# Optimization experiments

Measured on AMD Instinct MI355X. Metric: run time of the kernel, lower is better.

## Reference

```python
import jax, jax.numpy as jnp
import numpy as np
from jax import lax

THRESH = 0.6      # pnet score threshold (threshold[0])
IOU_THR = 0.5     # per-scale nms threshold in detect_face
K_PICKS = 128     # fixed max number of NMS picks (jit-static)
STRIDE = 2.0
CELL = 12.0
NEG = -1e30


def _conv(x, w, b):
    y = lax.conv_general_dilated(x, w, (1, 1), 'VALID',
                                 dimension_numbers=('NCHW', 'OIHW', 'NCHW'))
    return y + b[None, :, None, None]


def _prelu(x, a):
    return jnp.where(x > 0, x, a[None, :, None, None] * x)


def _maxpool2(x):
    return lax.reduce_window(x, -jnp.inf, lax.max, (1, 1, 2, 2), (1, 1, 2, 2), 'VALID')


def _nms(boxes, scores):
    # Greedy union-IoU NMS (nms_numpy math), vectorized with a fixed pick budget.
    # boxes [N,4] (shared grid), scores [N] with invalid entries already = NEG.
    x1, y1, x2, y2 = boxes[:, 0], boxes[:, 1], boxes[:, 2], boxes[:, 3]
    area = (x2 - x1 + 1.0) * (y2 - y1 + 1.0)

    def body(live, _):
        j = jnp.argmax(live)
        s = live[j]
        ok = s > NEG * 0.5
        xx1 = jnp.maximum(x1[j], x1); yy1 = jnp.maximum(y1[j], y1)
        xx2 = jnp.minimum(x2[j], x2); yy2 = jnp.minimum(y2[j], y2)
        inter = jnp.maximum(0.0, xx2 - xx1 + 1.0) * jnp.maximum(0.0, yy2 - yy1 + 1.0)
        iou = inter / (area[j] + area - inter)
        live = jnp.where(iou > IOU_THR, NEG, live).at[j].set(NEG)
        return live, (j, ok)

    _, (idx, ok) = lax.scan(body, scores, None, length=K_PICKS)
    return idx, ok


def setup_inputs():
    key = jax.random.key(0)
    ks = jax.random.split(key, 16)
    B, H, W = 16, 384, 512
    f = lambda k, shp, s=0.1: jax.random.normal(k, shp, jnp.float32) * s
    return {
        'im_data': jax.random.uniform(ks[0], (B, 3, H, W), jnp.float32) * 255.0,
        'c1_w': f(ks[1], (10, 3, 3, 3)), 'c1_b': f(ks[2], (10,)),
        'p1': jnp.full((10,), 0.25, jnp.float32),
        'c2_w': f(ks[3], (16, 10, 3, 3)), 'c2_b': f(ks[4], (16,)),
        'p2': jnp.full((16,), 0.25, jnp.float32),
        'c3_w': f(ks[5], (32, 16, 3, 3)), 'c3_b': f(ks[6], (32,)),
        'p3': jnp.full((32,), 0.25, jnp.float32),
        'c41_w': f(ks[7], (2, 32, 1, 1)), 'c41_b': f(ks[8], (2,)),
        'c42_w': f(ks[9], (4, 32, 1, 1)), 'c42_b': f(ks[10], (4,)),
    }


def reference(im_data, c1_w, c1_b, p1, c2_w, c2_b, p2, c3_w, c3_b, p3,
              c41_w, c41_b, c42_w, c42_b):
    # --- PNet conv trunk (detect_face normalization + MTCNN PNet) ---
    x = (im_data - 127.5) * 0.0078125
    h = _prelu(_conv(x, c1_w, c1_b), p1)
    h = _maxpool2(h)                                   # 2x2 s2 (dims even -> ceil==floor)
    h = _prelu(_conv(h, c2_w, c2_b), p2)
    h = _prelu(_conv(h, c3_w, c3_b), p3)
    probs = jax.nn.softmax(_conv(h, c41_w, c41_b), axis=1)[:, 1]   # [B,Hp,Wp]
    reg = _conv(h, c42_w, c42_b)                                   # [B,4,Hp,Wp]

    # --- generateBoundingBox (dense, masked instead of nonzero; scale=1) ---
    B, Hp, Wp = probs.shape
    yy, xx = jnp.meshgrid(jnp.arange(Hp, dtype=jnp.float32),
                          jnp.arange(Wp, dtype=jnp.float32), indexing='ij')
    boxes4 = jnp.stack([jnp.floor(STRIDE * xx + 1.0).ravel(),
                        jnp.floor(STRIDE * yy + 1.0).ravel(),
                        jnp.floor(STRIDE * xx + CELL).ravel(),
                        jnp.floor(STRIDE * yy + CELL).ravel()], axis=1)  # [N,4]
    scores = probs.reshape(B, -1)                                   # [B,N]
    regf = reg.reshape(B, 4, -1).transpose(0, 2, 1)                 # [B,N,4]
    masked = jnp.where(scores >= THRESH, scores, NEG)

    # --- per-image greedy NMS (batched_nms: images independent) ---
    idx, ok = jax.vmap(_nms, in_axes=(None, 0))(boxes4, masked)     # [B,K]
    pb = boxes4[idx]                                                # [B,K,4]
    ps = jnp.take_along_axis(scores, idx, axis=1)                   # [B,K]
    pr = jnp.take_along_axis(regf, idx[..., None], axis=1)          # [B,K,4]

    w = pb[..., 2] - pb[..., 0]
    hh = pb[..., 3] - pb[..., 1]
    q1 = pb[..., 0] + pr[..., 0] * w
    q2 = pb[..., 1] + pr[..., 1] * hh
    q3 = pb[..., 2] + pr[..., 2] * w
    q4 = pb[..., 3] + pr[..., 3] * hh
    rw = q3 - q1
    rh = q4 - q2
    l = jnp.maximum(rw, rh)
    nx1 = q1 + rw * 0.5 - l * 0.5
    ny1 = q2 + rh * 0.5 - l * 0.5
    out = jnp.stack([nx1, ny1, nx1 + l, ny1 + l, ps], axis=-1)      # [B,K,5]
    return out * ok[..., None].astype(out.dtype)
```

## Files before the change

kernel.cpp:

```cpp
#include <hip/hip_runtime.h>
#include <math.h>

#define BATCH 16
#define IH 384
#define IW 512
#define C1 10
#define P1H 191
#define P1W 255
#define C2 16
#define H2 189
#define W2 253
#define C3 32
#define H3 187
#define W3 251
#define N3 (H3*W3)
#define KP 128
#define CAP 7680
#define NEGV (-1e30f)

typedef _Float16 f16x8 __attribute__((ext_vector_type(8)));
typedef _Float16 f16x4 __attribute__((ext_vector_type(4)));
typedef float    f32x16 __attribute__((ext_vector_type(16)));

#define PXT 66
#define NSUB 2

#define T1R 34
#define T1C 68
__global__ __launch_bounds__(256, 1) void k_conv1pool(
        const float* __restrict__ im, const float* __restrict__ w,
        const float* __restrict__ bia, const float* __restrict__ slope,
        float* __restrict__ outp,
        const float* __restrict__ w3, _Float16* __restrict__ wbuf) {
    __shared__ float T[3 * T1R * T1C];

    int tx = threadIdx.x, ty = threadIdx.y;
    int tid = ty * 16 + tx;
    int bx = blockIdx.x, by = blockIdx.y, bb = blockIdx.z;

    if (bx == 0 && by == 0 && bb == 0) {
        for (int e = tid; e < 4608; e += 256) {
            int oc = e / 144;
            int rem = e - oc * 144;
            int ic = rem / 9;
            int tap = rem - ic * 9;
            float v = w3[e];
            _Float16 h = (_Float16)v;
            _Float16 l = (_Float16)(v - (float)h);
            int d = ((tap * 2 + (ic >> 3)) * 32 + oc) * 8 + (ic & 7);
            wbuf[d] = h;
            wbuf[4608 + d] = l;
        }
    }

    const size_t ibase = (size_t)bb * 3 * IH * IW;
    for (int g = tid; g < 3 * T1R * 33; g += 256) {
        int ch = g / (T1R * 33);
        int rem = g - ch * (T1R * 33);
        int r = rem / 33;
        int c2 = rem - r * 33;
        int yg = 32 * by + r;
        int xg = 64 * bx + 2 * c2;
        float2 v = make_float2(0.f, 0.f);
        if (yg < IH && xg < IW)
            v = *(const float2*)(im + ibase + ((size_t)ch * IH + yg) * IW + xg);
        float2 o;
        o.x = (v.x - 127.5f) * 0.0078125f;
        o.y = (v.y - 127.5f) * 0.0078125f;
        *(float2*)&T[(ch * T1R + r) * T1C + 2 * c2] = o;
    }
    __syncthreads();

    int Y  = by * 16 + ty;
    int X0 = bx * 32 + 2 * tx;
    if (Y >= P1H) return;

    float win[3][4][6];
    #pragma unroll
    for (int ch = 0; ch < 3; ++ch)
        #pragma unroll
        for (int r = 0; r < 4; ++r) {
            const float* p = &T[(ch * T1R + 2 * ty + r) * T1C + 4 * tx];
            float4 a = *(const float4*)p;
            float2 b = *(const float2*)(p + 4);
            win[ch][r][0] = a.x; win[ch][r][1] = a.y;
            win[ch][r][2] = a.z; win[ch][r][3] = a.w;
            win[ch][r][4] = b.x; win[ch][r][5] = b.y;
        }
    #pragma unroll
    for (int ch = 0; ch < 3; ++ch)
        #pragma unroll
        for (int r = 0; r < 4; ++r)
            #pragma unroll
            for (int c = 0; c < 6; ++c)
                asm volatile("" : "+v"(win[ch][r][c]));

    bool px1ok = (X0 + 1 < P1W);
    for (int oc = 0; oc < C1; ++oc) {
        const float* wo = w + oc * 27;
        float bv = bia[oc], sv = slope[oc];
        float c0 = bv, c1 = bv, c2 = bv, c3 = bv;
        float c4 = bv, c5 = bv, c6 = bv, c7 = bv;
        #pragma unroll
        for (int ch = 0; ch < 3; ++ch)
            #pragma unroll
            for (int ky = 0; ky < 3; ++ky)
                #pragma unroll
                for (int kx = 0; kx < 3; ++kx) {
                    float wv = wo[(ch * 3 + ky) * 3 + kx];
                    c0 += win[ch][0 + ky][0 + kx] * wv;
                    c1 += win[ch][0 + ky][1 + kx] * wv;
                    c2 += win[ch][0 + ky][2 + kx] * wv;
                    c3 += win[ch][0 + ky][3 + kx] * wv;
                    c4 += win[ch][1 + ky][0 + kx] * wv;
                    c5 += win[ch][1 + ky][1 + kx] * wv;
                    c6 += win[ch][1 + ky][2 + kx] * wv;
                    c7 += win[ch][1 + ky][3 + kx] * wv;
                }
        float m0 = fmaxf(fmaxf(c0, c1), fmaxf(c4, c5));
        float m1 = fmaxf(fmaxf(c2, c3), fmaxf(c6, c7));
        float p0 = m0 > 0.f ? m0 : sv * m0;
        float p1 = m1 > 0.f ? m1 : sv * m1;
        float* o = outp + (((size_t)bb * C1 + oc) * P1H + Y) * P1W + X0;
        o[0] = p0;
        if (px1ok) o[1] = p1;
    }
}

__global__ __launch_bounds__(256, 2) void k_conv2(
        const float* __restrict__ inp, const float* __restrict__ w,
        const float* __restrict__ bia, const float* __restrict__ slope,
        float* __restrict__ outp) {
    __shared__ __align__(16) float smem[8192];
    float* tile = smem;
    float4* sbuf = (float4*)smem;

    int tx = threadIdx.x, ty = threadIdx.y;
    int tid = ty * 64 + tx;
    int bx = blockIdx.x, byb = blockIdx.y, bb = blockIdx.z;

    const float* pin = inp + (size_t)bb * C1 * P1H * P1W;
    for (int g = tid; g < C1 * 6 * 130; g += 256) {
        int ic = g / 780;
        int rem = g - ic * 780;
        int r = rem / 130;
        int c = rem - r * 130;
        int yg = 4 * byb + r;
        int xg = 128 * bx + c;
        float v = 0.f;
        if (yg < P1H && xg < P1W)
            v = pin[((size_t)ic * P1H + yg) * P1W + xg];
        tile[(ic * 6 + r) * 132 + c] = v;
    }
    __syncthreads();

    int x0 = bx * 128 + tx * 2;
    int y  = byb * 4 + ty;
    bool alive = (x0 < W2) && (y < H2);

    float a0[C2], a1[C2];
    #pragma unroll
    for (int oc = 0; oc < C2; ++oc) { a0[oc] = bia[oc]; a1[oc] = bia[oc]; }

    if (alive) {
        for (int ci = 0; ci < C1; ++ci) {
            float v[3][4];
            #pragma unroll
            for (int r = 0; r < 3; ++r) {
                const float* p = &tile[(ci * 6 + ty + r) * 132 + 2 * tx];
                float2 u0 = *(const float2*)p;
                float2 u1 = *(const float2*)(p + 2);
                v[r][0] = u0.x; v[r][1] = u0.y; v[r][2] = u1.x; v[r][3] = u1.y;
            }
            const float* wc = w + ci * 9;
            #pragma unroll
            for (int oc = 0; oc < C2; ++oc) {
                const float* wo = wc + oc * (C1 * 9);
                float s0 = a0[oc], s1 = a1[oc];
                #pragma unroll
                for (int ky = 0; ky < 3; ++ky)
                    #pragma unroll
                    for (int kx = 0; kx < 3; ++kx) {
                        float wv = wo[ky * 3 + kx];
                        s0 += v[ky][kx]     * wv;
                        s1 += v[ky][kx + 1] * wv;
                    }
                a0[oc] = s0; a1[oc] = s1;
            }
        }
        #pragma unroll
        for (int oc = 0; oc < C2; ++oc) {
            float sl = slope[oc];
            float u0 = a0[oc]; a0[oc] = u0 > 0.f ? u0 : sl * u0;
            float u1 = a1[oc]; a1[oc] = u1 > 0.f ? u1 : sl * u1;
        }
    }
    __syncthreads();

    #pragma unroll
    for (int c4 = 0; c4 < 4; ++c4) {
        int g0 = tid * 8 + c4;
        int p0 = g0 ^ ((g0 >> 3) & 7);
        sbuf[p0] = make_float4(a0[c4 * 4], a0[c4 * 4 + 1], a0[c4 * 4 + 2], a0[c4 * 4 + 3]);
        int g1 = tid * 8 + 4 + c4;
        int p1 = g1 ^ ((g1 >> 3) & 7);
        sbuf[p1] = make_float4(a1[c4 * 4], a1[c4 * 4 + 1], a1[c4 * 4 + 2], a1[c4 * 4 + 3]);
    }
    __syncthreads();

    const size_t obase = (size_t)bb * H2 * W2 * C2;
    #pragma unroll
    for (int it = 0; it < 8; ++it) {
        int g = it * 256 + tid;
        int c4 = g & 3, px = (g >> 2) & 127, ry = g >> 9;
        int xg = blockIdx.x * 128 + px, yg = blockIdx.y * 4 + ry;
        if (xg < W2 && yg < H2) {
            int phys = g ^ ((g >> 3) & 7);
            *(float4*)(outp + obase + ((size_t)yg * W2 + xg) * C2 + c4 * 4) = sbuf[phys];
        }
    }
}

__global__ __launch_bounds__(256, 2) void k_conv3mfma(
        const float* __restrict__ act,
        const _Float16* __restrict__ wbuf,
        const float* __restrict__ b3, const float* __restrict__ s3,
        const float* __restrict__ w41, const float* __restrict__ b41,
        const float* __restrict__ w42, const float* __restrict__ b42,
        float* __restrict__ scores, float4* __restrict__ regf) {
    __shared__ __align__(16) _Float16 Ah[6 * 2 * PXT * 8];
    __shared__ __align__(16) _Float16 Al[6 * 2 * PXT * 8];
    __shared__ __align__(16) float    htab[32 * 8];

    int tid = threadIdx.x;
    int bx = blockIdx.x * (NSUB * 32);
    int by = blockIdx.y * 4;
    int bb = blockIdx.z;

    {
        int oc = tid >> 3, f = tid & 7;
        float v;
        if      (f == 0) v = b3[oc];
        else if (f == 1) v = s3[oc];
        else if (f == 2) v = w41[oc];
        else if (f == 3) v = w41[32 + oc];
        else             v = w42[(f - 4) * 32 + oc];
        htab[tid] = v;
    }
    {
        const float* actb = act + (size_t)bb * H2 * W2 * C2;
        for (int e = tid; e < 6 * PXT * 4; e += 256) {
            int ic4 = e & 3;
            int t = e >> 2;
            int px = t % PXT;
            int row = t / PXT;
            int yg = by + row, xg = bx + px;
            float4 v = make_float4(0.f, 0.f, 0.f, 0.f);
            if (yg < H2 && xg < W2)
                v = *(const float4*)(actb + ((size_t)yg * W2 + xg) * C2 + ic4 * 4);
            float xs0 = v.x, xs1 = v.y, xs2 = v.z, xs3 = v.w;
            f16x4 hv, lv;
            _Float16 h;
            h = (_Float16)xs0; hv[0] = h; lv[0] = (_Float16)(xs0 - (float)h);
            h = (_Float16)xs1; hv[1] = h; lv[1] = (_Float16)(xs1 - (float)h);
            h = (_Float16)xs2; hv[2] = h; lv[2] = (_Float16)(xs2 - (float)h);
            h = (_Float16)xs3; hv[3] = h; lv[3] = (_Float16)(xs3 - (float)h);
            int kg = ic4 >> 1, h4 = ic4 & 1;
            int gr = (row * 2 + kg) * PXT + px;
            *(f16x4*)(Ah + gr * 8 + h4 * 4) = hv;
            *(f16x4*)(Al + gr * 8 + h4 * 4) = lv;
        }
    }
    __syncthreads();

    int wv = tid >> 6, lane = tid & 63;
    int col = lane & 31, half = lane >> 5;
    int y = by + wv;
    if (y >= H3) return;

    f32x16 acc[NSUB];
    #pragma unroll
    for (int s = 0; s < NSUB; ++s)
        #pragma unroll
        for (int i = 0; i < 16; ++i) acc[s][i] = 0.f;

    const _Float16* wg = wbuf + (half * 32 + col) * 8;

    #pragma unroll 1
    for (int ky = 0; ky < 3; ++ky) {
        const _Float16* arh = Ah + ((wv + ky) * 2 + half) * (PXT * 8);
        const _Float16* arl = Al + ((wv + ky) * 2 + half) * (PXT * 8);
        #pragma unroll
        for (int kx = 0; kx < 3; ++kx) {
            int tap = ky * 3 + kx;
            f16x8 wh = *(const f16x8*)(wg + tap * 512);
            f16x8 wl = *(const f16x8*)(wg + 4608 + tap * 512);
            #pragma unroll
            for (int s = 0; s < NSUB; ++s) {
                int p = s * 32 + col + kx;
                f16x8 bh = *(const f16x8*)(arh + p * 8);
                f16x8 bl = *(const f16x8*)(arl + p * 8);
                acc[s] = __builtin_amdgcn_mfma_f32_32x32x16_f16(wh, bh, acc[s], 0, 0, 0);
                acc[s] = __builtin_amdgcn_mfma_f32_32x32x16_f16(wl, bh, acc[s], 0, 0, 0);
                acc[s] = __builtin_amdgcn_mfma_f32_32x32x16_f16(wh, bl, acc[s], 0, 0, 0);
            }
        }
    }

    float L0[NSUB], L1[NSUB], R0[NSUB], R1[NSUB], R2[NSUB], R3[NSUB];
    #pragma unroll
    for (int s = 0; s < NSUB; ++s) { L0[s]=0.f; L1[s]=0.f; R0[s]=0.f; R1[s]=0.f; R2[s]=0.f; R3[s]=0.f; }

    #pragma unroll
    for (int r = 0; r < 16; ++r) {
        int oc = (r & 3) + 8 * (r >> 2) + 4 * half;
        float4 t0 = *(const float4*)&htab[oc * 8];
        float4 t1 = *(const float4*)&htab[oc * 8 + 4];
        #pragma unroll
        for (int s = 0; s < NSUB; ++s) {
            float v = acc[s][r] + t0.x;
            v = v > 0.f ? v : v * t0.y;
            L0[s] += v * t0.z; L1[s] += v * t0.w;
            R0[s] += v * t1.x; R1[s] += v * t1.y;
            R2[s] += v * t1.z; R3[s] += v * t1.w;
        }
    }

    float hb0 = b41[0], hb1 = b41[1];
    float rb0 = b42[0], rb1 = b42[1], rb2 = b42[2], rb3 = b42[3];

    #pragma unroll
    for (int s = 0; s < NSUB; ++s) {
        float l0 = L0[s] + __shfl_xor(L0[s], 32) + hb0;
        float l1 = L1[s] + __shfl_xor(L1[s], 32) + hb1;
        float r0 = R0[s] + __shfl_xor(R0[s], 32) + rb0;
        float r1 = R1[s] + __shfl_xor(R1[s], 32) + rb1;
        float r2 = R2[s] + __shfl_xor(R2[s], 32) + rb2;
        float r3 = R3[s] + __shfl_xor(R3[s], 32) + rb3;
        float m = fmaxf(l0, l1);
        float e0 = expf(l0 - m), e1 = expf(l1 - m);
        float p = e1 / (e0 + e1);
        int px = bx + s * 32 + col;
        if (half == 0 && px < W3) {
            size_t n = (size_t)bb * N3 + (size_t)y * W3 + px;
            scores[n] = (p >= 0.6f) ? p : NEGV;
            regf[n] = make_float4(r0, r1, r2, r3);
        }
    }
}

__global__ __launch_bounds__(1024) void k_nms(
        const float* __restrict__ scores, const float4* __restrict__ regf,
        float* __restrict__ outp) {
    __shared__ float s_score[CAP];
    __shared__ int   s_idx[CAP];
    __shared__ float r_s[16];
    __shared__ int   r_i[16];
    __shared__ float s_picks[KP];
    __shared__ int   s_picki[KP];
    __shared__ int   s_misc[4];

    int tid = threadIdx.x;
    int bb = blockIdx.x;
    const float* sc = scores + (size_t)bb * N3;

    if (tid < 4) s_misc[tid] = 0;
    __syncthreads();

    int cnt = 0;
    for (int i = tid; i < N3; i += 1024) if (sc[i] > 0.f) cnt++;
    atomicAdd(&s_misc[0], cnt);
    __syncthreads();
    int M = s_misc[0];

    int cutbin = 0;
    if (M > CAP) {
        for (int i = tid; i < 2048; i += 1024) s_idx[i] = 0;
        __syncthreads();
        for (int i = tid; i < N3; i += 1024) {
            float s = sc[i];
            if (s > 0.f) {
                int b = (int)((s - 0.6f) * 5120.f);
                b = b < 0 ? 0 : (b > 2047 ? 2047 : b);
                atomicAdd(&s_idx[b], 1);
            }
        }
        __syncthreads();
        if (tid == 0) {
            int accum = 0, b = 2047;
            for (; b >= 0; --b) {
                int c = s_idx[b];
                if (accum + c > CAP) break;
                accum += c;
            }
            s_misc[2] = b + 1;
        }
        __syncthreads();
        cutbin = s_misc[2];
        __syncthreads();
    }

    for (int i = tid; i < N3; i += 1024) {
        float s = sc[i];
        if (s > 0.f) {
            bool keep = true;
            if (M > CAP) {
                int b = (int)((s - 0.6f) * 5120.f);
                b = b < 0 ? 0 : (b > 2047 ? 2047 : b);
                keep = (b >= cutbin);
            }
            if (keep) {
                int pos = atomicAdd(&s_misc[1], 1);
                if (pos < CAP) { s_score[pos] = s; s_idx[pos] = i; }
            }
        }
    }
    __syncthreads();
    int M2 = s_misc[1]; if (M2 > CAP) M2 = CAP;

    int np = 0;
    for (int pick = 0; pick < KP; ++pick) {
        float bs = -INFINITY; int bi = 0x7fffffff;
        for (int i = tid; i < M2; i += 1024) {
            float s = s_score[i]; int id = s_idx[i];
            if (s > bs || (s == bs && id < bi)) { bs = s; bi = id; }
        }
        #pragma unroll
        for (int off = 32; off; off >>= 1) {
            float os = __shfl_down(bs, off);
            int   oi = __shfl_down(bi, off);
            if (os > bs || (os == bs && oi < bi)) { bs = os; bi = oi; }
        }
        int lane = tid & 63, wv = tid >> 6;
        if (lane == 0) { r_s[wv] = bs; r_i[wv] = bi; }
        __syncthreads();
        if (tid == 0) {
            float ps = r_s[0]; int pi = r_i[0];
            for (int k = 1; k < 16; ++k) {
                float os = r_s[k]; int oi = r_i[k];
                if (os > ps || (os == ps && oi < pi)) { ps = os; pi = oi; }
            }
            s_picks[pick] = ps; s_picki[pick] = pi;
            r_s[0] = ps; r_i[0] = pi;
        }
        __syncthreads();
        float ps = r_s[0]; int pi = r_i[0];
        if (ps < 0.f) break;
        np = pick + 1;

        int pcx = pi % W3, pcy = pi / W3;
        float px1 = (float)(2 * pcx + 1), py1 = (float)(2 * pcy + 1);
        float px2 = (float)(2 * pcx + 12), py2 = (float)(2 * pcy + 12);
        for (int i = tid; i < M2; i += 1024) {
            float s = s_score[i];
            if (s > NEGV * 0.5f) {
                int id = s_idx[i];
                int cx = id % W3, cy = id / W3;
                float x1 = (float)(2 * cx + 1), y1 = (float)(2 * cy + 1);
                float x2 = (float)(2 * cx + 12), y2 = (float)(2 * cy + 12);
                float xx1 = fmaxf(px1, x1), yy1 = fmaxf(py1, y1);
                float xx2 = fminf(px2, x2), yy2 = fminf(py2, y2);
                float inter = fmaxf(0.f, xx2 - xx1 + 1.f) * fmaxf(0.f, yy2 - yy1 + 1.f);
                float iou = inter / (288.f - inter);
                if (iou > 0.5f) s_score[i] = NEGV;
            }
        }
        __syncthreads();
    }

    if (tid < KP) {
        float* o = outp + ((size_t)bb * KP + tid) * 5;
        if (tid < np) {
            int pi = s_picki[tid]; float ps = s_picks[tid];
            int cx = pi % W3, cy = pi / W3;
            float x1 = (float)(2 * cx + 1), y1 = (float)(2 * cy + 1);
            float x2 = (float)(2 * cx + 12), y2 = (float)(2 * cy + 12);
            float4 r = regf[(size_t)bb * N3 + pi];
            float wd = x2 - x1, hh = y2 - y1;
            float q1 = x1 + r.x * wd, q2 = y1 + r.y * hh;
            float q3 = x2 + r.z * wd, q4 = y2 + r.w * hh;
            float rw = q3 - q1, rh = q4 - q2;
            float L = fmaxf(rw, rh);
            float nx1 = q1 + rw * 0.5f - L * 0.5f;
            float ny1 = q2 + rh * 0.5f - L * 0.5f;
            o[0] = nx1; o[1] = ny1; o[2] = nx1 + L; o[3] = ny1 + L; o[4] = ps;
        } else {
            o[0] = 0.f; o[1] = 0.f; o[2] = 0.f; o[3] = 0.f; o[4] = 0.f;
        }
    }
}

extern "C" void kernel_launch(void* const* d_in, const int* in_sizes, int n_in,
                              void* d_out, int out_size, void* d_ws, size_t ws_size,
                              hipStream_t stream) {
    const float* im   = (const float*)d_in[0];
    const float* c1w  = (const float*)d_in[1];
    const float* c1b  = (const float*)d_in[2];
    const float* p1   = (const float*)d_in[3];
    const float* c2w  = (const float*)d_in[4];
    const float* c2b  = (const float*)d_in[5];
    const float* p2   = (const float*)d_in[6];
    const float* c3w  = (const float*)d_in[7];
    const float* c3b  = (const float*)d_in[8];
    const float* p3   = (const float*)d_in[9];
    const float* c41w = (const float*)d_in[10];
    const float* c41b = (const float*)d_in[11];
    const float* c42w = (const float*)d_in[12];
    const float* c42b = (const float*)d_in[13];

    float* ws = (float*)d_ws;
    const size_t POOL1_FLOATS = (size_t)BATCH * C1 * P1H * P1W;
    float*  pool1  = ws;
    float*  conv2b = ws + POOL1_FLOATS;
    float*  scoresb = ws;
    float4* regfb   = (float4*)(ws + (size_t)BATCH * N3);
    _Float16* wbuf = (_Float16*)d_out;

    k_conv1pool<<<dim3(8, 12, BATCH), dim3(16, 16), 0, stream>>>(im, c1w, c1b, p1, pool1,
                                                                 c3w, wbuf);
    k_conv2   <<<dim3(2, 48, BATCH), dim3(64, 4), 0, stream>>>(pool1, c2w, c2b, p2, conv2b);
    k_conv3mfma<<<dim3(4, 47, BATCH), dim3(256), 0, stream>>>(conv2b, wbuf, c3b, p3,
                                                              c41w, c41b, c42w, c42b,
                                                              scoresb, regfb);
    k_nms<<<dim3(BATCH), dim3(1024), 0, stream>>>(scoresb, regfb, (float*)d_out);
}
```

Before: 249.4 us.

## Fuse NMS suppression into next argmax pass and retune conv2 register allocation

The NMS loop now applies the previous pick's IoU suppression and the argmax scan in a single pass over the shared candidate list. This removes one shared-memory sweep and one barrier per pick, using double-buffered reduction slots to avoid a race. Separately, conv2 drops to one block per SIMD occupancy, disables unrolling of the input-channel loop, and pins the loaded window in registers with empty asm to limit register pressure and spills. The conv2 changes trade occupancy for fewer spills and may be neutral or negative.

```diff
diff --git a/kernel.cpp b/kernel.cpp
--- a/kernel.cpp
+++ b/kernel.cpp
@@ -127,7 +127,7 @@
     }
 }
 
-__global__ __launch_bounds__(256, 2) void k_conv2(
+__global__ __launch_bounds__(256, 1) void k_conv2(
         const float* __restrict__ inp, const float* __restrict__ w,
         const float* __restrict__ bia, const float* __restrict__ slope,
         float* __restrict__ outp) {
@@ -163,6 +163,7 @@
     for (int oc = 0; oc < C2; ++oc) { a0[oc] = bia[oc]; a1[oc] = bia[oc]; }
 
     if (alive) {
+        #pragma unroll 1
         for (int ci = 0; ci < C1; ++ci) {
             float v[3][4];
             #pragma unroll
@@ -172,6 +173,11 @@
                 float2 u1 = *(const float2*)(p + 2);
                 v[r][0] = u0.x; v[r][1] = u0.y; v[r][2] = u1.x; v[r][3] = u1.y;
             }
+            #pragma unroll
+            for (int r = 0; r < 3; ++r)
+                #pragma unroll
+                for (int k = 0; k < 4; ++k)
+                    asm volatile("" : "+v"(v[r][k]));
             const float* wc = w + ci * 9;
             #pragma unroll
             for (int oc = 0; oc < C2; ++oc) {
@@ -213,7 +219,7 @@
     for (int it = 0; it < 8; ++it) {
         int g = it * 256 + tid;
         int c4 = g & 3, px = (g >> 2) & 127, ry = g >> 9;
-        int xg = blockIdx.x * 128 + px, yg = blockIdx.y * 4 + ry;
+        int xg = bx * 128 + px, yg = byb * 4 + ry;
         if (xg < W2 && yg < H2) {
             int phys = g ^ ((g >> 3) & 7);
             *(float4*)(outp + obase + ((size_t)yg * W2 + xg) * C2 + c4 * 4) = sbuf[phys];
@@ -354,8 +360,8 @@
         float* __restrict__ outp) {
     __shared__ float s_score[CAP];
     __shared__ int   s_idx[CAP];
-    __shared__ float r_s[16];
-    __shared__ int   r_i[16];
+    __shared__ float r_s[2][16];
+    __shared__ int   r_i[2][16];
     __shared__ float s_picks[KP];
     __shared__ int   s_picki[KP];
     __shared__ int   s_misc[4];
@@ -419,41 +425,13 @@
     int M2 = s_misc[1]; if (M2 > CAP) M2 = CAP;
 
     int np = 0;
+    int   ppi = -1;
+    float px1 = 0.f, py1 = 0.f, px2 = 0.f, py2 = 0.f;
     for (int pick = 0; pick < KP; ++pick) {
         float bs = -INFINITY; int bi = 0x7fffffff;
         for (int i = tid; i < M2; i += 1024) {
-            float s = s_score[i]; int id = s_idx[i];
-            if (s > bs || (s == bs && id < bi)) { bs = s; bi = id; }
-        }
-        #pragma unroll
-        for (int off = 32; off; off >>= 1) {
-            float os = __shfl_down(bs, off);
-            int   oi = __shfl_down(bi, off);
-            if (os > bs || (os == bs && oi < bi)) { bs = os; bi = oi; }
-        }
-        int lane = tid & 63, wv = tid >> 6;
-        if (lane == 0) { r_s[wv] = bs; r_i[wv] = bi; }
-        __syncthreads();
-        if (tid == 0) {
-            float ps = r_s[0]; int pi = r_i[0];
-            for (int k = 1; k < 16; ++k) {
-                float os = r_s[k]; int oi = r_i[k];
-                if (os > ps || (os == ps && oi < pi)) { ps = os; pi = oi; }
-            }
-            s_picks[pick] = ps; s_picki[pick] = pi;
-            r_s[0] = ps; r_i[0] = pi;
-        }
-        __syncthreads();
-        float ps = r_s[0]; int pi = r_i[0];
-        if (ps < 0.f) break;
-        np = pick + 1;
-
-        int pcx = pi % W3, pcy = pi / W3;
-        float px1 = (float)(2 * pcx + 1), py1 = (float)(2 * pcy + 1);
-        float px2 = (float)(2 * pcx + 12), py2 = (float)(2 * pcy + 12);
-        for (int i = tid; i < M2; i += 1024) {
             float s = s_score[i];
-            if (s > NEGV * 0.5f) {
+            if (ppi >= 0 && s > NEGV * 0.5f) {
                 int id = s_idx[i];
                 int cx = id % W3, cy = id / W3;
                 float x1 = (float)(2 * cx + 1), y1 = (float)(2 * cy + 1);
@@ -462,10 +440,38 @@
                 float xx2 = fminf(px2, x2), yy2 = fminf(py2, y2);
                 float inter = fmaxf(0.f, xx2 - xx1 + 1.f) * fmaxf(0.f, yy2 - yy1 + 1.f);
                 float iou = inter / (288.f - inter);
-                if (iou > 0.5f) s_score[i] = NEGV;
-            }
-        }
+                if (iou > 0.5f) { s = NEGV; s_score[i] = NEGV; }
+            }
+            int id = s_idx[i];
+            if (s > bs || (s == bs && id < bi)) { bs = s; bi = id; }
+        }
+        #pragma unroll
+        for (int off = 32; off; off >>= 1) {
+            float os = __shfl_down(bs, off);
+            int   oi = __shfl_down(bi, off);
+            if (os > bs || (os == bs && oi < bi)) { bs = os; bi = oi; }
+        }
+        int lane = tid & 63, wv = tid >> 6, buf = pick & 1;
+        if (lane == 0) { r_s[buf][wv] = bs; r_i[buf][wv] = bi; }
         __syncthreads();
+        if (tid == 0) {
+            float ps = r_s[buf][0]; int pi = r_i[buf][0];
+            for (int k = 1; k < 16; ++k) {
+                float os = r_s[buf][k]; int oi = r_i[buf][k];
+                if (os > ps || (os == ps && oi < pi)) { ps = os; pi = oi; }
+            }
+            s_picks[pick] = ps; s_picki[pick] = pi;
+            r_s[buf][0] = ps; r_i[buf][0] = pi;
+        }
+        __syncthreads();
+        float ps = r_s[buf][0]; int pi = r_i[buf][0];
+        if (ps < 0.f) break;
+        np = pick + 1;
+
+        ppi = pi;
+        int pcx = pi % W3, pcy = pi / W3;
+        px1 = (float)(2 * pcx + 1);  py1 = (float)(2 * pcy + 1);
+        px2 = (float)(2 * pcx + 12); py2 = (float)(2 * pcy + 12);
     }
 
     if (tid < KP) {
```

Result: no change. 250.0 us (+0.2%).
